# Kernel optimization log

Measured on AMD Instinct MI355X. Metric: run time of the kernel, lower is better.

The kernel has to match this reference:

```python
import jax, jax.numpy as jnp
import numpy as np
from jax import lax

SEQ_LEN = 4096
INPUT_SIZE = 1024
HIDDEN = 1024
NUM_CLASSES = 3


def setup_inputs() -> dict:
    key = jax.random.key(0)
    ks = jax.random.split(key, 12)
    s = 1.0 / np.sqrt(HIDDEN)  # torch LSTM/Linear uniform init scale
    def u(k, shape):
        return jax.random.uniform(k, shape, jnp.float32, -s, s)
    inp = jax.random.normal(ks[0], (SEQ_LEN, 1, INPUT_SIZE), jnp.float32)
    return {
        "inp": inp,
        # forward-direction LSTM params (gate order i,f,g,o as in torch)
        "Wih_f": u(ks[1], (4 * HIDDEN, INPUT_SIZE)),
        "Whh_f": u(ks[2], (4 * HIDDEN, HIDDEN)),
        "bih_f": u(ks[3], (4 * HIDDEN,)),
        "bhh_f": u(ks[4], (4 * HIDDEN,)),
        # backward-direction LSTM params
        "Wih_b": u(ks[5], (4 * HIDDEN, INPUT_SIZE)),
        "Whh_b": u(ks[6], (4 * HIDDEN, HIDDEN)),
        "bih_b": u(ks[7], (4 * HIDDEN,)),
        "bhh_b": u(ks[8], (4 * HIDDEN,)),
        # output head: Linear(2*HIDDEN, 3)
        "W_ho": u(ks[9], (NUM_CLASSES, 2 * HIDDEN)),
        "b_ho": u(ks[10], (NUM_CLASSES,)),
    }


def _lstm_last_h(x, Wih, Whh, bih, bhh):
    # x: (T, B, I) -> final hidden state (B, H)
    H = Whh.shape[1]
    B = x.shape[1]
    bias = bih + bhh
    # precompute input projections for all timesteps: (T, B, 4H)
    xg = jnp.einsum('tbi,gi->tbg', x, Wih) + bias

    def step(carry, xt):
        h, c = carry
        gates = xt + h @ Whh.T  # (B, 4H)
        i, f, g, o = jnp.split(gates, 4, axis=-1)
        c = jax.nn.sigmoid(f) * c + jax.nn.sigmoid(i) * jnp.tanh(g)
        h = jax.nn.sigmoid(o) * jnp.tanh(c)
        return (h, c), None

    init = (jnp.zeros((B, H), x.dtype), jnp.zeros((B, H), x.dtype))
    (hT, _), _ = lax.scan(step, init, xg)
    return hT


def reference(inp, Wih_f, Whh_f, bih_f, bhh_f, Wih_b, Whh_b, bih_b, bhh_b, W_ho, b_ho):
    h_fwd = _lstm_last_h(inp, Wih_f, Whh_f, bih_f, bhh_f)          # (1, H)
    h_bwd = _lstm_last_h(inp[::-1], Wih_b, Whh_b, bih_b, bhh_b)    # (1, H)
    hidden = jnp.concatenate([h_fwd, h_bwd], axis=-1)              # (1, 2H)
    # Dropout(p=0.35) is identity in eval mode.
    return hidden @ W_ho.T + b_ho                                  # (1, 3)
```

## Files before the change

### kernel.cpp

```cpp
#include <hip/hip_runtime.h>
#include <stdint.h>


#define T_SEQ 4096
#define ISZ   1024
#define HID   1024
#define NB_TOT 256
#define NTHR  512

typedef unsigned long long u64;

__device__ __forceinline__ float fast_sigmoid(float x) {
    return 1.0f / (1.0f + __expf(-x));
}
__device__ __forceinline__ float fast_tanh(float x) {
    return 1.0f - 2.0f / (__expf(2.0f * x) + 1.0f);
}

#define PIN4(v) asm volatile("" : "+v"(v.x), "+v"(v.y), "+v"(v.z), "+v"(v.w))
#define DOT4(a, b) ((a).x*(b).x + (a).y*(b).y + (a).z*(b).z + (a).w*(b).w)

#define GM 64
#define GN 64
#define GK 32

__global__ __launch_bounds__(256)
void xproj_gemm(const float* __restrict__ x,
                const float* __restrict__ Wih_f, const float* __restrict__ bih_f,
                const float* __restrict__ bhh_f,
                const float* __restrict__ Wih_b, const float* __restrict__ bih_b,
                const float* __restrict__ bhh_b,
                float* __restrict__ xg)
{
    const int dir = blockIdx.z;
    const float* Wih = dir ? Wih_b : Wih_f;
    const float* bih = dir ? bih_b : bih_f;
    const float* bhh = dir ? bhh_b : bhh_f;
    const int m0 = blockIdx.y * GM;
    const int n0 = blockIdx.x * GN;
    const int tid = threadIdx.x;
    const int ms = tid >> 2;
    const int kq = tid & 3;
    const int tm = tid >> 4;
    const int tn = tid & 15;

    __shared__ float As[GK][GM + 4];
    __shared__ float Bs[GK][GN + 4];

    float acc[4][4] = {};

    const int mrow = m0 + ms;
    const int xrow = dir ? (T_SEQ - 1 - mrow) : mrow;
    const float* ap = x + (size_t)xrow * ISZ + kq * 8;
    const float* bp = Wih + (size_t)(n0 + ms) * ISZ + kq * 8;

    for (int k0 = 0; k0 < ISZ; k0 += GK) {
        float4 a0 = *(const float4*)(ap + k0);
        float4 a1 = *(const float4*)(ap + k0 + 4);
        float4 b0 = *(const float4*)(bp + k0);
        float4 b1 = *(const float4*)(bp + k0 + 4);
        __syncthreads();
        const int kb = kq * 8;
        As[kb+0][ms]=a0.x; As[kb+1][ms]=a0.y; As[kb+2][ms]=a0.z; As[kb+3][ms]=a0.w;
        As[kb+4][ms]=a1.x; As[kb+5][ms]=a1.y; As[kb+6][ms]=a1.z; As[kb+7][ms]=a1.w;
        Bs[kb+0][ms]=b0.x; Bs[kb+1][ms]=b0.y; Bs[kb+2][ms]=b0.z; Bs[kb+3][ms]=b0.w;
        Bs[kb+4][ms]=b1.x; Bs[kb+5][ms]=b1.y; Bs[kb+6][ms]=b1.z; Bs[kb+7][ms]=b1.w;
        __syncthreads();
        #pragma unroll
        for (int k = 0; k < GK; ++k) {
            float4 av = *(const float4*)&As[k][tm * 4];
            float4 bv = *(const float4*)&Bs[k][tn * 4];
            acc[0][0] += av.x*bv.x; acc[0][1] += av.x*bv.y; acc[0][2] += av.x*bv.z; acc[0][3] += av.x*bv.w;
            acc[1][0] += av.y*bv.x; acc[1][1] += av.y*bv.y; acc[1][2] += av.y*bv.z; acc[1][3] += av.y*bv.w;
            acc[2][0] += av.z*bv.x; acc[2][1] += av.z*bv.y; acc[2][2] += av.z*bv.z; acc[2][3] += av.z*bv.w;
            acc[3][0] += av.w*bv.x; acc[3][1] += av.w*bv.y; acc[3][2] += av.w*bv.z; acc[3][3] += av.w*bv.w;
        }
    }

    const int gc = n0 + tn * 4;
    float4 bb1 = *(const float4*)(bih + gc);
    float4 bb2 = *(const float4*)(bhh + gc);
    float bx = bb1.x + bb2.x, by = bb1.y + bb2.y, bz = bb1.z + bb2.z, bw = bb1.w + bb2.w;
    float* op = xg + ((size_t)dir << 24) + (size_t)(m0 + tm * 4) * 4096 + gc;
    #pragma unroll
    for (int i = 0; i < 4; ++i) {
        float4 v;
        v.x = acc[i][0] + bx; v.y = acc[i][1] + by;
        v.z = acc[i][2] + bz; v.w = acc[i][3] + bw;
        *(float4*)(op + (size_t)i * 4096) = v;
    }
}

__global__ __attribute__((amdgpu_flat_work_group_size(NTHR, NTHR)))
           __attribute__((amdgpu_waves_per_eu(2, 2)))
void bilstm_rec(const float* __restrict__ xg,
                const float* __restrict__ Whh_f, const float* __restrict__ Whh_b,
                u64* hpack)
{
    const int tid = threadIdx.x;
    const int blk = blockIdx.x;
    const int dir = blk >> 7;
    const int lb  = blk & 127;
    const int u0  = lb * 8;
    const int w   = tid >> 6;
    const int l   = tid & 63;
    const int unit = u0 + w;
    const int xsh = ((l >> 1) & 3) << 2;

    const float* Whh = dir ? Whh_b : Whh_f;
    const float* xgd = xg + ((size_t)dir << 24);
    u64* hp = hpack + (size_t)dir * 2 * HID;

    __shared__ __align__(16) float lds_h[2][HID];

    const float* wp0 = Whh + (size_t)(0 * HID + unit) * HID + l * 16;
    const float* wp1 = Whh + (size_t)(1 * HID + unit) * HID + l * 16;
    const float* wp2 = Whh + (size_t)(2 * HID + unit) * HID + l * 16;
    const float* wp3 = Whh + (size_t)(3 * HID + unit) * HID + l * 16;
    float4 w00 = *(const float4*)(wp0 + 0),  w01 = *(const float4*)(wp0 + 4);
    float4 w02 = *(const float4*)(wp0 + 8),  w03 = *(const float4*)(wp0 + 12);
    float4 w10 = *(const float4*)(wp1 + 0),  w11 = *(const float4*)(wp1 + 4);
    float4 w12 = *(const float4*)(wp1 + 8),  w13 = *(const float4*)(wp1 + 12);
    float4 w20 = *(const float4*)(wp2 + 0),  w21 = *(const float4*)(wp2 + 4);
    float4 w22 = *(const float4*)(wp2 + 8),  w23 = *(const float4*)(wp2 + 12);
    float4 w30 = *(const float4*)(wp3 + 0),  w31 = *(const float4*)(wp3 + 4);
    float4 w32 = *(const float4*)(wp3 + 8),  w33 = *(const float4*)(wp3 + 12);
    PIN4(w00); PIN4(w01); PIN4(w02); PIN4(w03);
    PIN4(w10); PIN4(w11); PIN4(w12); PIN4(w13);
    PIN4(w20); PIN4(w21); PIN4(w22); PIN4(w23);
    PIN4(w30); PIN4(w31); PIN4(w32); PIN4(w33);

    float c_state = 0.0f;
    float xgv = 0.0f;
    if (l < 4) xgv = xgd[(size_t)l * HID + unit];
    asm volatile("" : "+v"(xgv));

    bool dead = false;

    for (int t = 0; t < T_SEQ; ++t) {
        float s0 = 0.f, s1 = 0.f, s2 = 0.f, s3 = 0.f;

        if (t > 0) {
            const int b = (t - 1) & 1;
            u64* src = hp + (size_t)b * HID;
            const int k0 = tid * 2;
            u64 e0 = 0, e1 = 0;
            if (!dead) {
                int sp = 0;
                for (;;) {
                    e0 = __hip_atomic_load(src + k0,     __ATOMIC_RELAXED,
                                           __HIP_MEMORY_SCOPE_AGENT);
                    e1 = __hip_atomic_load(src + k0 + 1, __ATOMIC_RELAXED,
                                           __HIP_MEMORY_SCOPE_AGENT);
                    if (((unsigned)(e0 >> 32) == (unsigned)t) &
                        ((unsigned)(e1 >> 32) == (unsigned)t)) break;
                    if (++sp > (1 << 21)) { dead = true; break; }
                    __builtin_amdgcn_s_sleep(1);
                }
            }
            const int mi = (k0 & ~15) | ((k0 & 15) ^ (((k0 >> 5) & 3) << 2));
            float2 hv;
            hv.x = __uint_as_float((unsigned)(e0 & 0xffffffffu));
            hv.y = __uint_as_float((unsigned)(e1 & 0xffffffffu));
            *(float2*)&lds_h[b][mi] = hv;
            __syncthreads();

            const float* lh = &lds_h[b][l * 16];
            float4 h0 = *(const float4*)(lh + (0  ^ xsh));
            float4 h1 = *(const float4*)(lh + (4  ^ xsh));
            float4 h2 = *(const float4*)(lh + (8  ^ xsh));
            float4 h3 = *(const float4*)(lh + (12 ^ xsh));

            s0 = DOT4(w00,h0) + DOT4(w01,h1) + DOT4(w02,h2) + DOT4(w03,h3);
            s1 = DOT4(w10,h0) + DOT4(w11,h1) + DOT4(w12,h2) + DOT4(w13,h3);
            s2 = DOT4(w20,h0) + DOT4(w21,h1) + DOT4(w22,h2) + DOT4(w23,h3);
            s3 = DOT4(w30,h0) + DOT4(w31,h1) + DOT4(w32,h2) + DOT4(w33,h3);
        }

        #pragma unroll
        for (int m = 1; m < 64; m <<= 1) {
            s0 += __shfl_xor(s0, m);
            s1 += __shfl_xor(s1, m);
            s2 += __shfl_xor(s2, m);
            s3 += __shfl_xor(s3, m);
        }

        float xg1 = __shfl(xgv, 1);
        float xg2 = __shfl(xgv, 2);
        float xg3 = __shfl(xgv, 3);

        if (l == 0) {
            float gi = s0 + xgv;
            float gf = s1 + xg1;
            float gg = s2 + xg2;
            float go = s3 + xg3;
            float si = fast_sigmoid(gi);
            float sf = fast_sigmoid(gf);
            float tg = fast_tanh(gg);
            float so = fast_sigmoid(go);
            c_state = sf * c_state + si * tg;
            float hval = so * fast_tanh(c_state);
            u64 pk = ((u64)(unsigned)(t + 1) << 32) | (u64)__float_as_uint(hval);
            __hip_atomic_store(hp + (size_t)(t & 1) * HID + unit, pk,
                               __ATOMIC_RELAXED, __HIP_MEMORY_SCOPE_AGENT);
        }

        if (t + 1 < T_SEQ && l < 4) {
            xgv = xgd[(size_t)(t + 1) * 4096 + (size_t)l * HID + unit];
            asm volatile("" : "+v"(xgv));
        }
    }
}

__global__ void head_kernel(const float* __restrict__ W_ho,
                            const float* __restrict__ b_ho,
                            const u64* __restrict__ hpack,
                            float* __restrict__ out)
{
    const u64* hf  = hpack + 1 * HID;
    const u64* hbk = hpack + 2 * HID + 1 * HID;
    __shared__ float r0[4], r1[4], r2[4];
    int tid = threadIdx.x;
    float p0 = 0.f, p1 = 0.f, p2 = 0.f;
    for (int i = tid; i < 2 * HID; i += 256) {
        u64 e = (i < HID) ? hf[i] : hbk[i - HID];
        float hv = __uint_as_float((unsigned)(e & 0xffffffffu));
        p0 += W_ho[0 * 2 * HID + i] * hv;
        p1 += W_ho[1 * 2 * HID + i] * hv;
        p2 += W_ho[2 * 2 * HID + i] * hv;
    }
    #pragma unroll
    for (int m = 1; m < 64; m <<= 1) {
        p0 += __shfl_xor(p0, m);
        p1 += __shfl_xor(p1, m);
        p2 += __shfl_xor(p2, m);
    }
    int w = tid >> 6;
    if ((tid & 63) == 0) { r0[w] = p0; r1[w] = p1; r2[w] = p2; }
    __syncthreads();
    if (tid == 0) {
        out[0] = b_ho[0] + r0[0] + r0[1] + r0[2] + r0[3];
        out[1] = b_ho[1] + r1[0] + r1[1] + r1[2] + r1[3];
        out[2] = b_ho[2] + r2[0] + r2[1] + r2[2] + r2[3];
    }
}

extern "C" void kernel_launch(void* const* d_in, const int* in_sizes, int n_in,
                              void* d_out, int out_size, void* d_ws, size_t ws_size,
                              hipStream_t stream) {
    const float* x     = (const float*)d_in[0];
    const float* Wih_f = (const float*)d_in[1];
    const float* Whh_f = (const float*)d_in[2];
    const float* bih_f = (const float*)d_in[3];
    const float* bhh_f = (const float*)d_in[4];
    const float* Wih_b = (const float*)d_in[5];
    const float* Whh_b = (const float*)d_in[6];
    const float* bih_b = (const float*)d_in[7];
    const float* bhh_b = (const float*)d_in[8];
    const float* W_ho  = (const float*)d_in[9];
    const float* b_ho  = (const float*)d_in[10];

    u64* hpack = (u64*)d_ws;
    float* xg = (float*)((char*)d_ws + 32768);

    hipMemsetAsync(d_ws, 0, 2 * 2 * HID * sizeof(u64), stream);

    dim3 gg(4096 / GN, T_SEQ / GM, 2);
    xproj_gemm<<<gg, 256, 0, stream>>>(x, Wih_f, bih_f, bhh_f,
                                       Wih_b, bih_b, bhh_b, xg);
    bilstm_rec<<<NB_TOT, NTHR, 0, stream>>>(xg, Whh_f, Whh_b, hpack);
    head_kernel<<<1, 256, 0, stream>>>(W_ho, b_ho, hpack, (float*)d_out);
}
```

Measured before the change: 8.990 ms.

## Split each wave into four gate groups with 64-wide k-chunks

Remaps lanes so each 16-lane quarter of a wave computes one gate row over 64-element k-chunks, instead of every lane computing partial sums for all four gates. The cross-lane reduction shrinks from six shuffle rounds on four values to four rounds on one value. Gate activations are computed in parallel across quarters, with tanh written as a scaled sigmoid. The LDS h buffer is padded to stride 68 to limit bank conflicts, and each lane now reads 64 h values from LDS instead of 16, which raises LDS traffic per step.

```diff
diff --git a/kernel.cpp b/kernel.cpp
--- a/kernel.cpp
+++ b/kernel.cpp
@@ -7,6 +7,7 @@
 #define HID   1024
 #define NB_TOT 256
 #define NTHR  512
+#define PAD   68
 
 typedef unsigned long long u64;
 
@@ -104,41 +105,44 @@
     const int u0  = lb * 8;
     const int w   = tid >> 6;
     const int l   = tid & 63;
+    const int q   = l >> 4;
+    const int kc  = l & 15;
     const int unit = u0 + w;
-    const int xsh = ((l >> 1) & 3) << 2;
+    const int grow = q * HID + unit;
 
     const float* Whh = dir ? Whh_b : Whh_f;
     const float* xgd = xg + ((size_t)dir << 24);
     u64* hp = hpack + (size_t)dir * 2 * HID;
 
-    __shared__ __align__(16) float lds_h[2][HID];
-
-    const float* wp0 = Whh + (size_t)(0 * HID + unit) * HID + l * 16;
-    const float* wp1 = Whh + (size_t)(1 * HID + unit) * HID + l * 16;
-    const float* wp2 = Whh + (size_t)(2 * HID + unit) * HID + l * 16;
-    const float* wp3 = Whh + (size_t)(3 * HID + unit) * HID + l * 16;
-    float4 w00 = *(const float4*)(wp0 + 0),  w01 = *(const float4*)(wp0 + 4);
-    float4 w02 = *(const float4*)(wp0 + 8),  w03 = *(const float4*)(wp0 + 12);
-    float4 w10 = *(const float4*)(wp1 + 0),  w11 = *(const float4*)(wp1 + 4);
-    float4 w12 = *(const float4*)(wp1 + 8),  w13 = *(const float4*)(wp1 + 12);
-    float4 w20 = *(const float4*)(wp2 + 0),  w21 = *(const float4*)(wp2 + 4);
-    float4 w22 = *(const float4*)(wp2 + 8),  w23 = *(const float4*)(wp2 + 12);
-    float4 w30 = *(const float4*)(wp3 + 0),  w31 = *(const float4*)(wp3 + 4);
-    float4 w32 = *(const float4*)(wp3 + 8),  w33 = *(const float4*)(wp3 + 12);
-    PIN4(w00); PIN4(w01); PIN4(w02); PIN4(w03);
-    PIN4(w10); PIN4(w11); PIN4(w12); PIN4(w13);
-    PIN4(w20); PIN4(w21); PIN4(w22); PIN4(w23);
-    PIN4(w30); PIN4(w31); PIN4(w32); PIN4(w33);
+    __shared__ __align__(16) float lds_h[2][16 * PAD];
+
+    const float* wp = Whh + (size_t)grow * HID + kc * 64;
+    float4 w0 = *(const float4*)(wp + 0),  w1 = *(const float4*)(wp + 4);
+    float4 w2 = *(const float4*)(wp + 8),  w3 = *(const float4*)(wp + 12);
+    float4 w4 = *(const float4*)(wp + 16), w5 = *(const float4*)(wp + 20);
+    float4 w6 = *(const float4*)(wp + 24), w7 = *(const float4*)(wp + 28);
+    float4 w8 = *(const float4*)(wp + 32), w9 = *(const float4*)(wp + 36);
+    float4 wa = *(const float4*)(wp + 40), wb = *(const float4*)(wp + 44);
+    float4 wc = *(const float4*)(wp + 48), wd = *(const float4*)(wp + 52);
+    float4 we = *(const float4*)(wp + 56), wf = *(const float4*)(wp + 60);
+    PIN4(w0); PIN4(w1); PIN4(w2); PIN4(w3);
+    PIN4(w4); PIN4(w5); PIN4(w6); PIN4(w7);
+    PIN4(w8); PIN4(w9); PIN4(wa); PIN4(wb);
+    PIN4(wc); PIN4(wd); PIN4(we); PIN4(wf);
+
+    const float a_scl = (q == 2) ? 2.0f : 1.0f;
+    const float a_mul = (q == 2) ? 2.0f : 1.0f;
+    const float a_add = (q == 2) ? -1.0f : 0.0f;
 
     float c_state = 0.0f;
     float xgv = 0.0f;
-    if (l < 4) xgv = xgd[(size_t)l * HID + unit];
+    if (kc == 0) xgv = xgd[grow];
     asm volatile("" : "+v"(xgv));
 
     bool dead = false;
 
     for (int t = 0; t < T_SEQ; ++t) {
-        float s0 = 0.f, s1 = 0.f, s2 = 0.f, s3 = 0.f;
+        float s = 0.0f;
 
         if (t > 0) {
             const int b = (t - 1) & 1;
@@ -158,46 +162,41 @@
                     __builtin_amdgcn_s_sleep(1);
                 }
             }
-            const int mi = (k0 & ~15) | ((k0 & 15) ^ (((k0 >> 5) & 3) << 2));
             float2 hv;
             hv.x = __uint_as_float((unsigned)(e0 & 0xffffffffu));
             hv.y = __uint_as_float((unsigned)(e1 & 0xffffffffu));
-            *(float2*)&lds_h[b][mi] = hv;
+            *(float2*)&lds_h[b][(k0 >> 6) * PAD + (k0 & 63)] = hv;
             __syncthreads();
 
-            const float* lh = &lds_h[b][l * 16];
-            float4 h0 = *(const float4*)(lh + (0  ^ xsh));
-            float4 h1 = *(const float4*)(lh + (4  ^ xsh));
-            float4 h2 = *(const float4*)(lh + (8  ^ xsh));
-            float4 h3 = *(const float4*)(lh + (12 ^ xsh));
-
-            s0 = DOT4(w00,h0) + DOT4(w01,h1) + DOT4(w02,h2) + DOT4(w03,h3);
-            s1 = DOT4(w10,h0) + DOT4(w11,h1) + DOT4(w12,h2) + DOT4(w13,h3);
-            s2 = DOT4(w20,h0) + DOT4(w21,h1) + DOT4(w22,h2) + DOT4(w23,h3);
-            s3 = DOT4(w30,h0) + DOT4(w31,h1) + DOT4(w32,h2) + DOT4(w33,h3);
-        }
-
-        #pragma unroll
-        for (int m = 1; m < 64; m <<= 1) {
-            s0 += __shfl_xor(s0, m);
-            s1 += __shfl_xor(s1, m);
-            s2 += __shfl_xor(s2, m);
-            s3 += __shfl_xor(s3, m);
-        }
-
-        float xg1 = __shfl(xgv, 1);
-        float xg2 = __shfl(xgv, 2);
-        float xg3 = __shfl(xgv, 3);
+            const float* lh = &lds_h[b][kc * PAD];
+            float4 h0 = *(const float4*)(lh + 0),  h1 = *(const float4*)(lh + 4);
+            float4 h2 = *(const float4*)(lh + 8),  h3 = *(const float4*)(lh + 12);
+            float4 h4 = *(const float4*)(lh + 16), h5 = *(const float4*)(lh + 20);
+            float4 h6 = *(const float4*)(lh + 24), h7 = *(const float4*)(lh + 28);
+            s  = DOT4(w0,h0) + DOT4(w1,h1) + DOT4(w2,h2) + DOT4(w3,h3);
+            s += DOT4(w4,h4) + DOT4(w5,h5) + DOT4(w6,h6) + DOT4(w7,h7);
+            float4 h8 = *(const float4*)(lh + 32), h9 = *(const float4*)(lh + 36);
+            float4 ha = *(const float4*)(lh + 40), hb = *(const float4*)(lh + 44);
+            float4 hc = *(const float4*)(lh + 48), hd = *(const float4*)(lh + 52);
+            float4 he = *(const float4*)(lh + 56), hf = *(const float4*)(lh + 60);
+            s += DOT4(w8,h8) + DOT4(w9,h9) + DOT4(wa,ha) + DOT4(wb,hb);
+            s += DOT4(wc,hc) + DOT4(wd,hd) + DOT4(we,he) + DOT4(wf,hf);
+        }
+
+        s += __shfl_xor(s, 1);
+        s += __shfl_xor(s, 2);
+        s += __shfl_xor(s, 4);
+        s += __shfl_xor(s, 8);
+
+        float pg = s + xgv;
+        float act = a_mul * fast_sigmoid(a_scl * pg) + a_add;
+
+        float sf = __shfl(act, 16);
+        float tg = __shfl(act, 32);
+        float so = __shfl(act, 48);
 
         if (l == 0) {
-            float gi = s0 + xgv;
-            float gf = s1 + xg1;
-            float gg = s2 + xg2;
-            float go = s3 + xg3;
-            float si = fast_sigmoid(gi);
-            float sf = fast_sigmoid(gf);
-            float tg = fast_tanh(gg);
-            float so = fast_sigmoid(go);
+            float si = act;
             c_state = sf * c_state + si * tg;
             float hval = so * fast_tanh(c_state);
             u64 pk = ((u64)(unsigned)(t + 1) << 32) | (u64)__float_as_uint(hval);
@@ -205,8 +204,8 @@
                                __ATOMIC_RELAXED, __HIP_MEMORY_SCOPE_AGENT);
         }
 
-        if (t + 1 < T_SEQ && l < 4) {
-            xgv = xgd[(size_t)(t + 1) * 4096 + (size_t)l * HID + unit];
+        if (t + 1 < T_SEQ && kc == 0) {
+            xgv = xgd[(size_t)(t + 1) * 4096 + grow];
             asm volatile("" : "+v"(xgv));
         }
     }
```

Result: faster. 7.994 ms (-11.1%).
